# Kernel tuning notes

Hardware: AMD Instinct MI355X
Metric: run time of the kernel (lower is better)

Reference implementation:

```python
import jax, jax.numpy as jnp
import numpy as np

NUM_HEADS = 8

def _mha(x, in_w, in_b, out_w, out_b):
    # x: [B, L, E]; in_w: [3E, E]; out_w: [E, E]
    B, L, E = x.shape
    H = NUM_HEADS
    Dh = E // H
    qkv = x @ in_w.T + in_b                      # [B, L, 3E]
    q, k, v = jnp.split(qkv, 3, axis=-1)
    # [B, H, L, Dh]
    q = q.reshape(B, L, H, Dh).transpose(0, 2, 1, 3)
    k = k.reshape(B, L, H, Dh).transpose(0, 2, 1, 3)
    v = v.reshape(B, L, H, Dh).transpose(0, 2, 1, 3)
    scale = 1.0 / jnp.sqrt(jnp.asarray(Dh, dtype=x.dtype))
    scores = jnp.einsum('bhld,bhsd->bhls', q, k) * scale   # [B, H, L, S]
    attn = jax.nn.softmax(scores, axis=-1)
    ctx = jnp.einsum('bhls,bhsd->bhld', attn, v)           # [B, H, L, Dh]
    ctx = ctx.transpose(0, 2, 1, 3).reshape(B, L, E)
    out = ctx @ out_w.T + out_b                             # [B, L, E]
    # PyTorch default average_attn_weights=True: mean over heads -> [B, L, S]
    weights = attn.mean(axis=1)
    return out, weights

def setup_inputs() -> dict:
    key = jax.random.key(0)
    ks = jax.random.split(key, 5)
    B, L, E = 4, 2048, 1024
    s = 0.02
    return {
        'hidden_states': jax.random.normal(ks[0], (B, L, E), dtype=jnp.float32),
        'in_proj_w': jax.random.normal(ks[1], (3 * E, E), dtype=jnp.float32) * s,
        'in_proj_b': jnp.zeros((3 * E,), dtype=jnp.float32),
        'out_proj_w': jax.random.normal(ks[2], (E, E), dtype=jnp.float32) * s,
        'out_proj_b': jnp.zeros((E,), dtype=jnp.float32),
        'dep_proj_w': jax.random.normal(ks[3], (E, E), dtype=jnp.float32) * s,
        'dep_proj_b': jnp.zeros((E,), dtype=jnp.float32),
    }

def reference(hidden_states, in_proj_w, in_proj_b, out_proj_w, out_proj_b, dep_proj_w, dep_proj_b):
    enhanced, attn_weights = _mha(hidden_states, in_proj_w, in_proj_b, out_proj_w, out_proj_b)
    # dependency_scores: mean over query dim then key dim -> [B]
    dependency_scores = attn_weights.mean(axis=1).mean(axis=-1)
    enhanced = enhanced @ dep_proj_w.T + dep_proj_b
    return dependency_scores, enhanced
```

## Files before the change

kernel.cpp:

```cpp
#include <hip/hip_runtime.h>


typedef __attribute__((ext_vector_type(8))) short short8;
typedef __attribute__((ext_vector_type(4))) float float4v;
typedef __attribute__((ext_vector_type(4))) int int4v;
typedef __attribute__((ext_vector_type(2))) unsigned uint2v;

__device__ inline ushort f2bf(float f) {
  union { float f; unsigned u; } v; v.f = f;
  unsigned u = v.u;
  return (ushort)((u + 0x7FFFu + ((u >> 16) & 1u)) >> 16);
}
__device__ inline float bf2f(ushort h) {
  union { unsigned u; float f; } v; v.u = ((unsigned)h) << 16;
  return v.f;
}
__device__ inline unsigned cvtpk(float lo, float hi) {
  unsigned r;
  asm("v_cvt_pk_bf16_f32 %0, %1, %2" : "=v"(r) : "v"(lo), "v"(hi));
  return r;
}

__global__ __launch_bounds__(256)
void prep(const float* __restrict__ X, const float* __restrict__ Wi,
          const float* __restrict__ Wd, const float* __restrict__ Wo,
          const float* __restrict__ bo, const float* __restrict__ bd,
          ushort* __restrict__ Xb, ushort* __restrict__ Wib,
          ushort* __restrict__ Wdb, ushort* __restrict__ WoT,
          float* __restrict__ bc, float* __restrict__ dep) {
  __shared__ ushort Ts[64 * 72];
  const int bid = blockIdx.x;
  const int t = threadIdx.x;

  if (bid < 6144) {
    size_t i = ((size_t)bid * 256 + t) * 8;
    const float* src; ushort* dst;
    if (i < 8388608)        { src = X  + i;              dst = Xb  + i; }
    else if (i < 11534336)  { src = Wi + (i - 8388608);  dst = Wib + (i - 8388608); }
    else                    { src = Wd + (i - 11534336); dst = Wdb + (i - 11534336); }
    float4v a = *(const float4v*)(src);
    float4v b = *(const float4v*)(src + 4);
    ushort o[8];
    o[0] = f2bf(a.x); o[1] = f2bf(a.y); o[2] = f2bf(a.z); o[3] = f2bf(a.w);
    o[4] = f2bf(b.x); o[5] = f2bf(b.y); o[6] = f2bf(b.z); o[7] = f2bf(b.w);
    *(int4v*)dst = *(const int4v*)o;
  } else if (bid < 6400) {
    const int q = bid - 6144;
    const int ct = (q & 15) * 64, rt = (q >> 4) * 64;
#pragma unroll
    for (int i = 0; i < 4; i++) {
      const int row = i * 16 + (t >> 4), col4 = (t & 15) * 4;
      float4v v = *(const float4v*)(Wo + (size_t)(rt + row) * 1024 + ct + col4);
      ushort o[4] = {f2bf(v.x), f2bf(v.y), f2bf(v.z), f2bf(v.w)};
      *(uint2v*)(Ts + row * 72 + col4) = *(const uint2v*)o;
    }
    __syncthreads();
#pragma unroll
    for (int it = 0; it < 2; it++) {
      const int c = it * 256 + t;
      const int oc = c >> 3, r8 = (c & 7) * 8;
      ushort o[8];
#pragma unroll
      for (int j = 0; j < 8; j++) o[j] = Ts[(r8 + j) * 72 + oc];
      *(int4v*)(WoT + (size_t)(ct + oc) * 1024 + rt + r8) = *(const int4v*)o;
    }
  } else {
    const int w = t >> 6, lane = t & 63;
    const int row = (bid - 6400) * 4 + w;
    float s = 0.f;
#pragma unroll
    for (int i = 0; i < 4; i++) {
      const int j = i * 256 + lane * 4;
      float4v wv = *(const float4v*)(Wd + (size_t)row * 1024 + j);
      float4v bv = *(const float4v*)(bo + j);
      s += wv.x * bv.x + wv.y * bv.y + wv.z * bv.z + wv.w * bv.w;
    }
#pragma unroll
    for (int off = 1; off <= 32; off <<= 1) s += __shfl_xor(s, off);
    if (lane == 0) bc[row] = s + bd[row];
    if (row < 4 && lane == 1) dep[row] = 1.0f / 2048.0f;
  }
}

__global__ __launch_bounds__(256, 2)
void gemm_bt(const ushort* __restrict__ A, const ushort* __restrict__ W,
             ushort* __restrict__ C, int K) {
  __shared__ ushort As[128 * 32];
  __shared__ ushort Bs[128 * 32];
  const int t = threadIdx.x;
  const int w = t >> 6;
  const int lane = t & 63;
  const int m16 = lane & 15, quad = lane >> 4;
  const int bx = blockIdx.x, by = blockIdx.y;
  const int warpRow = w >> 1, warpCol = w & 1;

  const int srow = t >> 2;
  const int scol = (t & 3) * 8;
  const ushort* Aptr = A + (size_t)(by * 128) * K;
  const ushort* Wptr = W + (size_t)(bx * 128) * K;

  float4v zero4 = {0.f, 0.f, 0.f, 0.f};
  float4v acc[4][4];
#pragma unroll
  for (int i = 0; i < 4; i++)
#pragma unroll
    for (int j = 0; j < 4; j++) acc[i][j] = zero4;

  for (int k0 = 0; k0 < K; k0 += 32) {
    __syncthreads();
#pragma unroll
    for (int r = 0; r < 2; r++) {
      const ushort* g = Aptr + (size_t)(r * 64 + srow) * K + (k0 + scol);
      __builtin_amdgcn_global_load_lds(
          (const __attribute__((address_space(1))) void*)g,
          (__attribute__((address_space(3))) void*)(As + r * 2048 + t * 8),
          16, 0, 0);
    }
#pragma unroll
    for (int r = 0; r < 2; r++) {
      const ushort* g = Wptr + (size_t)(r * 64 + srow) * K + (k0 + scol);
      __builtin_amdgcn_global_load_lds(
          (const __attribute__((address_space(1))) void*)g,
          (__attribute__((address_space(3))) void*)(Bs + r * 2048 + t * 8),
          16, 0, 0);
    }
    __syncthreads();

    short8 af[4], bf[4];
#pragma unroll
    for (int i = 0; i < 4; i++) {
      af[i] = *(const short8*)(As + (warpRow * 64 + i * 16 + m16) * 32 + quad * 8);
      bf[i] = *(const short8*)(Bs + (warpCol * 64 + i * 16 + m16) * 32 + quad * 8);
    }
#pragma unroll
    for (int i = 0; i < 4; i++)
#pragma unroll
      for (int j = 0; j < 4; j++)
        acc[i][j] = __builtin_amdgcn_mfma_f32_16x16x32_bf16(af[i], bf[j],
                                                            acc[i][j], 0, 0, 0);
  }

  const int crow_base = by * 128 + warpRow * 64;
  const int ccol_base = bx * 128 + warpCol * 64;
#pragma unroll
  for (int j = 0; j < 4; j++) {
    const int col = ccol_base + j * 16 + m16;
#pragma unroll
    for (int i = 0; i < 4; i++) {
      const int row = crow_base + i * 16 + quad * 4;
#pragma unroll
      for (int r = 0; r < 4; r++)
        C[(size_t)(row + r) * 1024 + col] = f2bf(acc[i][j][r]);
    }
  }
}

__global__ __launch_bounds__(256, 2)
void gemm_qkv(const ushort* __restrict__ Xb, const ushort* __restrict__ Wib,
              const float* __restrict__ bi, ushort* __restrict__ qkv,
              ushort* __restrict__ Vt,
              const ushort* __restrict__ A2, const ushort* __restrict__ W2,
              ushort* __restrict__ C2) {
  __shared__ ushort As[128 * 32];
  __shared__ ushort Bs[128 * 32];
  const int t = threadIdx.x;
  const int w = t >> 6;
  const int lane = t & 63;
  const int m16 = lane & 15, quad = lane >> 4;
  const int bid = blockIdx.x;
  const bool second = bid >= 1536;
  int bx, by;
  const ushort *A, *W;
  if (!second) {
    const int swz = (bid & 7) * 192 + (bid >> 3);
    bx = swz % 24; by = swz / 24; A = Xb; W = Wib;
  } else {
    const int b2 = bid - 1536; bx = b2 & 7; by = b2 >> 3; A = A2; W = W2;
  }
  const int warpRow = w >> 1, warpCol = w & 1;
  const int K = 1024;

  const int srow = t >> 2;
  const int scol = (t & 3) * 8;
  const ushort* Aptr = A + (size_t)(by * 128) * K;
  const ushort* Wptr = W + (size_t)(bx * 128) * K;

  float4v zero4 = {0.f, 0.f, 0.f, 0.f};
  float4v acc[4][4];
#pragma unroll
  for (int i = 0; i < 4; i++)
#pragma unroll
    for (int j = 0; j < 4; j++) acc[i][j] = zero4;

  for (int k0 = 0; k0 < K; k0 += 32) {
    __syncthreads();
#pragma unroll
    for (int r = 0; r < 2; r++) {
      const ushort* g = Aptr + (size_t)(r * 64 + srow) * K + (k0 + scol);
      __builtin_amdgcn_global_load_lds(
          (const __attribute__((address_space(1))) void*)g,
          (__attribute__((address_space(3))) void*)(As + r * 2048 + t * 8),
          16, 0, 0);
    }
#pragma unroll
    for (int r = 0; r < 2; r++) {
      const ushort* g = Wptr + (size_t)(r * 64 + srow) * K + (k0 + scol);
      __builtin_amdgcn_global_load_lds(
          (const __attribute__((address_space(1))) void*)g,
          (__attribute__((address_space(3))) void*)(Bs + r * 2048 + t * 8),
          16, 0, 0);
    }
    __syncthreads();

    short8 af[4], bf[4];
#pragma unroll
    for (int i = 0; i < 4; i++) {
      af[i] = *(const short8*)(As + (warpRow * 64 + i * 16 + m16) * 32 + quad * 8);
      bf[i] = *(const short8*)(Bs + (warpCol * 64 + i * 16 + m16) * 32 + quad * 8);
    }
#pragma unroll
    for (int i = 0; i < 4; i++)
#pragma unroll
      for (int j = 0; j < 4; j++)
        acc[i][j] = __builtin_amdgcn_mfma_f32_16x16x32_bf16(af[i], bf[j],
                                                            acc[i][j], 0, 0, 0);
  }

  const int crow_base = by * 128 + warpRow * 64;
  const int ccol_base = bx * 128 + warpCol * 64;

  if (second) {
#pragma unroll
    for (int j = 0; j < 4; j++) {
      const int col = ccol_base + j * 16 + m16;
#pragma unroll
      for (int i = 0; i < 4; i++) {
        const int row = crow_base + i * 16 + quad * 4;
#pragma unroll
        for (int r = 0; r < 4; r++)
          C2[(size_t)(row + r) * 1024 + col] = f2bf(acc[i][j][r]);
      }
    }
  } else if (bx < 16) {
#pragma unroll
    for (int j = 0; j < 4; j++) {
      const int col = ccol_base + j * 16 + m16;
      const float bv = bi[col];
#pragma unroll
      for (int i = 0; i < 4; i++) {
        const int row = crow_base + i * 16 + quad * 4;
#pragma unroll
        for (int r = 0; r < 4; r++)
          qkv[(size_t)(row + r) * 3072 + col] = f2bf(acc[i][j][r] + bv);
      }
    }
  } else {
    const int b = by >> 4;
#pragma unroll
    for (int j = 0; j < 4; j++) {
      const int col = ccol_base + j * 16 + m16;
      const float bv = bi[col];
      const int vcol = col - 2048;
      const int h = vcol >> 7, d = vcol & 127;
      ushort* vrow = Vt + (size_t)((b * 8 + h) * 128 + d) * 2048;
#pragma unroll
      for (int i = 0; i < 4; i++) {
        const int pos = ((by & 15) << 7) + warpRow * 64 + ((i >> 1) << 5) +
                        (2 * quad + (i & 1)) * 4;
        uint2v o;
        o.x = cvtpk(acc[i][j][0] + bv, acc[i][j][1] + bv);
        o.y = cvtpk(acc[i][j][2] + bv, acc[i][j][3] + bv);
        *(uint2v*)(vrow + pos) = o;
      }
    }
  }
}

__global__ __launch_bounds__(512, 1)
void attn(const ushort* __restrict__ qkv, const ushort* __restrict__ Vt,
          ushort* __restrict__ ctx) {
  __shared__ ushort Ks[4][32 * 128];
  __shared__ ushort Vsm[4][128 * 32];
  const int t = threadIdx.x, w = t >> 6, lane = t & 63;
  const int m16 = lane & 15, quad = lane >> 4;
  const int i = blockIdx.x;
  const int x = i & 7, jj0 = i >> 3;
  const int pair = x * 4 + (jj0 >> 3);
  const int qt = jj0 & 7;
  const int h = pair & 7, b = pair >> 3;
  const int E3 = 3072;
  const size_t bbase = (size_t)b * 2048;

  const ushort* Qg = qkv + (bbase + qt * 256 + w * 32) * E3 + h * 128;
  const ushort* Kg = qkv + bbase * E3 + 1024 + h * 128;
  const ushort* Vg = Vt + (size_t)((b * 8 + h) * 128) * 2048;

  auto stage = [&](int kt, int buf) {
    {
      const int row = t >> 4, cir = t & 15;
      const int j = (cir & 8) | ((cir ^ row) & 7);
      const ushort* g = Kg + (size_t)(kt * 32 + row) * E3 + j * 8;
      __builtin_amdgcn_global_load_lds(
          (const __attribute__((address_space(1))) void*)g,
          (__attribute__((address_space(3))) void*)(&Ks[buf][t * 8]), 16, 0, 0);
    }
    {
      const int d = t >> 2, cir = t & 3;
      const int j = cir ^ ((d >> 1) & 3);
      const ushort* g = Vg + (size_t)d * 2048 + kt * 32 + j * 8;
      __builtin_amdgcn_global_load_lds(
          (const __attribute__((address_space(1))) void*)g,
          (__attribute__((address_space(3))) void*)(&Vsm[buf][t * 8]), 16, 0, 0);
    }
  };

  stage(0, 0);
  stage(1, 1);

  const float c1 = 0.08838834764831845f * 1.4426950408889634f;
  short8 qf[2][4];
#pragma unroll
  for (int g = 0; g < 2; g++)
#pragma unroll
    for (int ks = 0; ks < 4; ks++) {
      short8 raw = *(const short8*)(Qg + (size_t)(g * 16 + m16) * E3 + ks * 32 + quad * 8);
      short8 s;
#pragma unroll
      for (int j = 0; j < 8; j++) s[j] = (short)f2bf(bf2f((ushort)raw[j]) * c1);
      qf[g][ks] = s;
    }

  int kslot[4];
#pragma unroll
  for (int ks = 0; ks < 4; ks++) {
    const int j = ks * 4 + quad;
    kslot[ks] = (j & 8) | ((j ^ m16) & 7);
  }
  const int vslot = quad ^ ((m16 >> 1) & 3);

  float4v zero4 = {0.f, 0.f, 0.f, 0.f};
  float4v Oacc[2][8];
#pragma unroll
  for (int g = 0; g < 2; g++)
#pragma unroll
    for (int dt = 0; dt < 8; dt++) Oacc[g][dt] = zero4;
  float lsum[2] = {0.f, 0.f};

  for (int kt = 0; kt < 64; kt++) {
    if (kt < 62) {
      stage(kt + 2, (kt + 2) & 3);
      asm volatile("s_waitcnt vmcnt(4)" ::: "memory");
    } else if (kt == 62) {
      asm volatile("s_waitcnt vmcnt(2)" ::: "memory");
    } else {
      asm volatile("s_waitcnt vmcnt(0)" ::: "memory");
    }
    __builtin_amdgcn_s_barrier();
    __builtin_amdgcn_sched_barrier(0);
    const ushort* Ksb = Ks[kt & 3];
    const ushort* Vsb = Vsm[kt & 3];

    float4v st[2][2];
    st[0][0] = zero4; st[0][1] = zero4; st[1][0] = zero4; st[1][1] = zero4;
    __builtin_amdgcn_s_setprio(1);
#pragma unroll
    for (int ks = 0; ks < 4; ks++) {
#pragma unroll
      for (int mt2 = 0; mt2 < 2; mt2++) {
        short8 kf = *(const short8*)(Ksb + (mt2 * 16 + m16) * 128 + kslot[ks] * 8);
        st[0][mt2] = __builtin_amdgcn_mfma_f32_16x16x32_bf16(kf, qf[0][ks], st[0][mt2], 0, 0, 0);
        st[1][mt2] = __builtin_amdgcn_mfma_f32_16x16x32_bf16(kf, qf[1][ks], st[1][mt2], 0, 0, 0);
      }
    }
    __builtin_amdgcn_s_setprio(0);

    short8 pfr[2];
#pragma unroll
    for (int g = 0; g < 2; g++) {
      unsigned pk[4];
#pragma unroll
      for (int mt2 = 0; mt2 < 2; mt2++) {
        float p0 = __builtin_exp2f(st[g][mt2][0]);
        float p1 = __builtin_exp2f(st[g][mt2][1]);
        float p2 = __builtin_exp2f(st[g][mt2][2]);
        float p3 = __builtin_exp2f(st[g][mt2][3]);
        lsum[g] += (p0 + p1) + (p2 + p3);
        pk[mt2 * 2]     = cvtpk(p0, p1);
        pk[mt2 * 2 + 1] = cvtpk(p2, p3);
      }
      union { int4v i; short8 s; } pf;
      pf.i.x = (int)pk[0];
      pf.i.y = (int)pk[1];
      pf.i.z = (int)pk[2];
      pf.i.w = (int)pk[3];
      pfr[g] = pf.s;
    }

    __builtin_amdgcn_s_setprio(1);
#pragma unroll
    for (int dt = 0; dt < 8; dt++) {
      short8 vf = *(const short8*)(Vsb + (dt * 16 + m16) * 32 + vslot * 8);
      Oacc[0][dt] = __builtin_amdgcn_mfma_f32_16x16x32_bf16(pfr[0], vf, Oacc[0][dt], 0, 0, 0);
      Oacc[1][dt] = __builtin_amdgcn_mfma_f32_16x16x32_bf16(pfr[1], vf, Oacc[1][dt], 0, 0, 0);
    }
    __builtin_amdgcn_s_setprio(0);
  }

#pragma unroll
  for (int g = 0; g < 2; g++) {
    float l = lsum[g];
    l += __shfl_xor(l, 16);
    l += __shfl_xor(l, 32);
    float* lf = (float*)(&Ks[0][w * 64]);
    lf[m16] = l;
    float linv[4];
#pragma unroll
    for (int r = 0; r < 4; r++) linv[r] = 1.0f / lf[quad * 4 + r];
#pragma unroll
    for (int r = 0; r < 4; r++) {
      const int row = qt * 256 + w * 32 + g * 16 + quad * 4 + r;
      ushort* crow = ctx + (bbase + row) * 1024 + h * 128;
#pragma unroll
      for (int dt = 0; dt < 8; dt++)
        crow[dt * 16 + m16] = f2bf(Oacc[g][dt][r] * linv[r]);
    }
  }
}

__global__ __launch_bounds__(256, 2)
void gemm_fin(const ushort* __restrict__ A, const ushort* __restrict__ W,
              const float* __restrict__ bias, float* __restrict__ C) {
  __shared__ ushort As[128 * 32];
  __shared__ ushort Bs[128 * 32];
  const int t = threadIdx.x;
  const int w = t >> 6;
  const int lane = t & 63;
  const int m16 = lane & 15, quad = lane >> 4;
  const int swz = (blockIdx.x & 7) * 64 + (blockIdx.x >> 3);
  const int bx = swz & 7, by = swz >> 3;
  const int warpRow = w >> 1, warpCol = w & 1;
  const int K = 1024;

  const int srow = t >> 2;
  const int scol = (t & 3) * 8;
  const ushort* Aptr = A + (size_t)(by * 128) * K;
  const ushort* Wptr = W + (size_t)(bx * 128) * K;

  float4v zero4 = {0.f, 0.f, 0.f, 0.f};
  float4v acc[4][4];
#pragma unroll
  for (int i = 0; i < 4; i++)
#pragma unroll
    for (int j = 0; j < 4; j++) acc[i][j] = zero4;

  for (int k0 = 0; k0 < K; k0 += 32) {
    __syncthreads();
#pragma unroll
    for (int r = 0; r < 2; r++) {
      const ushort* g = Aptr + (size_t)(r * 64 + srow) * K + (k0 + scol);
      __builtin_amdgcn_global_load_lds(
          (const __attribute__((address_space(1))) void*)g,
          (__attribute__((address_space(3))) void*)(As + r * 2048 + t * 8),
          16, 0, 0);
    }
#pragma unroll
    for (int r = 0; r < 2; r++) {
      const ushort* g = Wptr + (size_t)(r * 64 + srow) * K + (k0 + scol);
      __builtin_amdgcn_global_load_lds(
          (const __attribute__((address_space(1))) void*)g,
          (__attribute__((address_space(3))) void*)(Bs + r * 2048 + t * 8),
          16, 0, 0);
    }
    __syncthreads();

    short8 af[4], bf[4];
#pragma unroll
    for (int i = 0; i < 4; i++) {
      af[i] = *(const short8*)(As + (warpRow * 64 + i * 16 + m16) * 32 + quad * 8);
      bf[i] = *(const short8*)(Bs + (warpCol * 64 + i * 16 + m16) * 32 + quad * 8);
    }
#pragma unroll
    for (int i = 0; i < 4; i++)
#pragma unroll
      for (int j = 0; j < 4; j++)
        acc[i][j] = __builtin_amdgcn_mfma_f32_16x16x32_bf16(af[i], bf[j],
                                                            acc[i][j], 0, 0, 0);
  }

  const int crow_base = by * 128 + warpRow * 64;
  const int ccol_base = bx * 128 + warpCol * 64;
#pragma unroll
  for (int j = 0; j < 4; j++) {
    const int col = ccol_base + j * 16 + m16;
    const float bv = bias[col];
#pragma unroll
    for (int i = 0; i < 4; i++) {
      const int row = crow_base + i * 16 + quad * 4;
#pragma unroll
      for (int r = 0; r < 4; r++)
        C[(size_t)(row + r) * 1024 + col] = acc[i][j][r] + bv;
    }
  }
}

extern "C" void kernel_launch(void* const* d_in, const int* in_sizes, int n_in,
                              void* d_out, int out_size, void* d_ws, size_t ws_size,
                              hipStream_t stream) {
  const float* X  = (const float*)d_in[0];
  const float* Wi = (const float*)d_in[1];
  const float* bi = (const float*)d_in[2];
  const float* Wo = (const float*)d_in[3];
  const float* bo = (const float*)d_in[4];
  const float* Wd = (const float*)d_in[5];
  const float* bd = (const float*)d_in[6];
  float* out = (float*)d_out;

  ushort* p    = (ushort*)d_ws;
  ushort* Xb   = p; p += (size_t)8192 * 1024;
  ushort* Wib  = p; p += (size_t)3072 * 1024;
  ushort* WoTb = p; p += (size_t)1024 * 1024;
  ushort* Wdb  = p; p += (size_t)1024 * 1024;
  ushort* qkv  = p; p += (size_t)8192 * 3072;
  ushort* Vt   = p; p += (size_t)4096 * 2048;
  float*  bc   = (float*)p; p += 2048;
  ushort* WcbSep = p; p += (size_t)1024 * 1024;
  const size_t need_merged = (size_t)((char*)p - (char*)d_ws);
  const bool merged = ws_size >= need_merged;

  ushort* ctx = Xb;
  ushort* Wcb = merged ? WcbSep : Wib;

  prep<<<6656, 256, 0, stream>>>(X, Wi, Wd, Wo, bo, bd,
                                 Xb, Wib, Wdb, WoTb, bc, out);
  if (merged) {
    gemm_qkv<<<1600, 256, 0, stream>>>(Xb, Wib, bi, qkv, Vt, Wdb, WoTb, Wcb);
  } else {
    gemm_qkv<<<1536, 256, 0, stream>>>(Xb, Wib, bi, qkv, Vt, Wdb, WoTb, nullptr);
    gemm_bt<<<dim3(8, 8), 256, 0, stream>>>(Wdb, WoTb, Wcb, 1024);
  }
  attn<<<256, 512, 0, stream>>>(qkv, Vt, ctx);
  gemm_fin<<<512, 256, 0, stream>>>(ctx, Wcb, bc, out + 4);
}
```

Baseline: 287.3 us.

## Restructure attention into 2-wave blocks with 64 query rows per wave

The attention kernel goes from 512-thread blocks of 8 waves, each handling 32 query rows, to 128-thread blocks of 2 waves, each handling 64 query rows. The grid doubles to 512 blocks. Each wave now reuses every K and V fragment loaded from LDS across four query groups instead of two, and each thread issues four times as many async global-to-LDS loads per stage, so the vmcnt waits are raised to match. This cuts LDS read traffic per MFMA and spreads work over more blocks, at the cost of more registers (larger Q and O accumulators) and fewer waves per block to hide latency.

```diff
diff --git a/kernel.cpp b/kernel.cpp
--- a/kernel.cpp
+++ b/kernel.cpp
@@ -276,7 +276,7 @@
   }
 }
 
-__global__ __launch_bounds__(512, 1)
+__global__ __launch_bounds__(128, 1)
 void attn(const ushort* __restrict__ qkv, const ushort* __restrict__ Vt,
           ushort* __restrict__ ctx) {
   __shared__ ushort Ks[4][32 * 128];
@@ -284,33 +284,37 @@
   const int t = threadIdx.x, w = t >> 6, lane = t & 63;
   const int m16 = lane & 15, quad = lane >> 4;
   const int i = blockIdx.x;
-  const int x = i & 7, jj0 = i >> 3;
-  const int pair = x * 4 + (jj0 >> 3);
-  const int qt = jj0 & 7;
+  const int x = i & 7, r0 = i >> 3;
+  const int pair = x * 4 + (r0 >> 4);
+  const int qt = r0 & 15;
   const int h = pair & 7, b = pair >> 3;
   const int E3 = 3072;
   const size_t bbase = (size_t)b * 2048;
 
-  const ushort* Qg = qkv + (bbase + qt * 256 + w * 32) * E3 + h * 128;
+  const ushort* Qg = qkv + (bbase + qt * 128 + w * 64) * E3 + h * 128;
   const ushort* Kg = qkv + bbase * E3 + 1024 + h * 128;
   const ushort* Vg = Vt + (size_t)((b * 8 + h) * 128) * 2048;
 
   auto stage = [&](int kt, int buf) {
-    {
-      const int row = t >> 4, cir = t & 15;
+#pragma unroll
+    for (int it = 0; it < 4; it++) {
+      const int c = it * 128 + t;
+      const int row = c >> 4, cir = c & 15;
       const int j = (cir & 8) | ((cir ^ row) & 7);
       const ushort* g = Kg + (size_t)(kt * 32 + row) * E3 + j * 8;
       __builtin_amdgcn_global_load_lds(
           (const __attribute__((address_space(1))) void*)g,
-          (__attribute__((address_space(3))) void*)(&Ks[buf][t * 8]), 16, 0, 0);
-    }
-    {
-      const int d = t >> 2, cir = t & 3;
+          (__attribute__((address_space(3))) void*)(&Ks[buf][c * 8]), 16, 0, 0);
+    }
+#pragma unroll
+    for (int it = 0; it < 4; it++) {
+      const int c = it * 128 + t;
+      const int d = c >> 2, cir = c & 3;
       const int j = cir ^ ((d >> 1) & 3);
       const ushort* g = Vg + (size_t)d * 2048 + kt * 32 + j * 8;
       __builtin_amdgcn_global_load_lds(
           (const __attribute__((address_space(1))) void*)g,
-          (__attribute__((address_space(3))) void*)(&Vsm[buf][t * 8]), 16, 0, 0);
+          (__attribute__((address_space(3))) void*)(&Vsm[buf][c * 8]), 16, 0, 0);
     }
   };
 
@@ -318,9 +322,9 @@
   stage(1, 1);
 
   const float c1 = 0.08838834764831845f * 1.4426950408889634f;
-  short8 qf[2][4];
-#pragma unroll
-  for (int g = 0; g < 2; g++)
+  short8 qf[4][4];
+#pragma unroll
+  for (int g = 0; g < 4; g++)
 #pragma unroll
     for (int ks = 0; ks < 4; ks++) {
       short8 raw = *(const short8*)(Qg + (size_t)(g * 16 + m16) * E3 + ks * 32 + quad * 8);
@@ -339,19 +343,19 @@
   const int vslot = quad ^ ((m16 >> 1) & 3);
 
   float4v zero4 = {0.f, 0.f, 0.f, 0.f};
-  float4v Oacc[2][8];
-#pragma unroll
-  for (int g = 0; g < 2; g++)
+  float4v Oacc[4][8];
+#pragma unroll
+  for (int g = 0; g < 4; g++)
 #pragma unroll
     for (int dt = 0; dt < 8; dt++) Oacc[g][dt] = zero4;
-  float lsum[2] = {0.f, 0.f};
+  float lsum[4] = {0.f, 0.f, 0.f, 0.f};
 
   for (int kt = 0; kt < 64; kt++) {
     if (kt < 62) {
       stage(kt + 2, (kt + 2) & 3);
-      asm volatile("s_waitcnt vmcnt(4)" ::: "memory");
+      asm volatile("s_waitcnt vmcnt(16)" ::: "memory");
     } else if (kt == 62) {
-      asm volatile("s_waitcnt vmcnt(2)" ::: "memory");
+      asm volatile("s_waitcnt vmcnt(8)" ::: "memory");
     } else {
       asm volatile("s_waitcnt vmcnt(0)" ::: "memory");
     }
@@ -360,23 +364,25 @@
     const ushort* Ksb = Ks[kt & 3];
     const ushort* Vsb = Vsm[kt & 3];
 
-    float4v st[2][2];
-    st[0][0] = zero4; st[0][1] = zero4; st[1][0] = zero4; st[1][1] = zero4;
+    float4v st[4][2];
+#pragma unroll
+    for (int g = 0; g < 4; g++) { st[g][0] = zero4; st[g][1] = zero4; }
     __builtin_amdgcn_s_setprio(1);
 #pragma unroll
     for (int ks = 0; ks < 4; ks++) {
 #pragma unroll
       for (int mt2 = 0; mt2 < 2; mt2++) {
         short8 kf = *(const short8*)(Ksb + (mt2 * 16 + m16) * 128 + kslot[ks] * 8);
-        st[0][mt2] = __builtin_amdgcn_mfma_f32_16x16x32_bf16(kf, qf[0][ks], st[0][mt2], 0, 0, 0);
-        st[1][mt2] = __builtin_amdgcn_mfma_f32_16x16x32_bf16(kf, qf[1][ks], st[1][mt2], 0, 0, 0);
+#pragma unroll
+        for (int g = 0; g < 4; g++)
+          st[g][mt2] = __builtin_amdgcn_mfma_f32_16x16x32_bf16(kf, qf[g][ks], st[g][mt2], 0, 0, 0);
       }
     }
     __builtin_amdgcn_s_setprio(0);
 
-    short8 pfr[2];
-#pragma unroll
-    for (int g = 0; g < 2; g++) {
+    short8 pfr[4];
+#pragma unroll
+    for (int g = 0; g < 4; g++) {
       unsigned pk[4];
 #pragma unroll
       for (int mt2 = 0; mt2 < 2; mt2++) {
@@ -400,14 +406,15 @@
 #pragma unroll
     for (int dt = 0; dt < 8; dt++) {
       short8 vf = *(const short8*)(Vsb + (dt * 16 + m16) * 32 + vslot * 8);
-      Oacc[0][dt] = __builtin_amdgcn_mfma_f32_16x16x32_bf16(pfr[0], vf, Oacc[0][dt], 0, 0, 0);
-      Oacc[1][dt] = __builtin_amdgcn_mfma_f32_16x16x32_bf16(pfr[1], vf, Oacc[1][dt], 0, 0, 0);
+#pragma unroll
+      for (int g = 0; g < 4; g++)
+        Oacc[g][dt] = __builtin_amdgcn_mfma_f32_16x16x32_bf16(pfr[g], vf, Oacc[g][dt], 0, 0, 0);
     }
     __builtin_amdgcn_s_setprio(0);
   }
 
 #pragma unroll
-  for (int g = 0; g < 2; g++) {
+  for (int g = 0; g < 4; g++) {
     float l = lsum[g];
     l += __shfl_xor(l, 16);
     l += __shfl_xor(l, 32);
@@ -418,7 +425,7 @@
     for (int r = 0; r < 4; r++) linv[r] = 1.0f / lf[quad * 4 + r];
 #pragma unroll
     for (int r = 0; r < 4; r++) {
-      const int row = qt * 256 + w * 32 + g * 16 + quad * 4 + r;
+      const int row = qt * 128 + w * 64 + g * 16 + quad * 4 + r;
       ushort* crow = ctx + (bbase + row) * 1024 + h * 128;
 #pragma unroll
       for (int dt = 0; dt < 8; dt++)
@@ -538,6 +545,6 @@
     gemm_qkv<<<1536, 256, 0, stream>>>(Xb, Wib, bi, qkv, Vt, Wdb, WoTb, nullptr);
     gemm_bt<<<dim3(8, 8), 256, 0, stream>>>(Wdb, WoTb, Wcb, 1024);
   }
-  attn<<<256, 512, 0, stream>>>(qkv, Vt, ctx);
+  attn<<<512, 128, 0, stream>>>(qkv, Vt, ctx);
   gemm_fin<<<512, 256, 0, stream>>>(ctx, Wcb, bc, out + 4);
 }
```

New measurement: 310.6 us. 1.08x slower.

## Replace LDS-staged attention with single-wave blocks loading K/V directly into registers

Applied to the files above, without the earlier changes.

The attention kernel moves from 512-thread blocks that share K/V tiles through a 4-deep LDS ring with barriers to 64-thread single-wave blocks. Each wave now loads its own K and V fragments from global memory into registers, prefetching the next tile (K double-buffered, V reloaded after use), and the row-sum broadcast uses shuffles instead of LDS. This removes block barriers and LDS traffic. In exchange, every wave re-reads the full K/V for its head, raising global and L2 traffic about eightfold, and it adds register pressure.

```diff
diff --git a/kernel.cpp b/kernel.cpp
--- a/kernel.cpp
+++ b/kernel.cpp
@@ -276,46 +276,37 @@
   }
 }
 
-__global__ __launch_bounds__(512, 1)
+__global__ __launch_bounds__(64, 2)
 void attn(const ushort* __restrict__ qkv, const ushort* __restrict__ Vt,
           ushort* __restrict__ ctx) {
-  __shared__ ushort Ks[4][32 * 128];
-  __shared__ ushort Vsm[4][128 * 32];
-  const int t = threadIdx.x, w = t >> 6, lane = t & 63;
+  const int lane = threadIdx.x;
   const int m16 = lane & 15, quad = lane >> 4;
   const int i = blockIdx.x;
-  const int x = i & 7, jj0 = i >> 3;
-  const int pair = x * 4 + (jj0 >> 3);
-  const int qt = jj0 & 7;
+  const int x = i & 7, j0 = i >> 3;
+  const int pair = x * 4 + (j0 >> 6);
+  const int qw = j0 & 63;
   const int h = pair & 7, b = pair >> 3;
   const int E3 = 3072;
   const size_t bbase = (size_t)b * 2048;
 
-  const ushort* Qg = qkv + (bbase + qt * 256 + w * 32) * E3 + h * 128;
+  const ushort* Qg = qkv + (bbase + qw * 32) * E3 + h * 128;
   const ushort* Kg = qkv + bbase * E3 + 1024 + h * 128;
   const ushort* Vg = Vt + (size_t)((b * 8 + h) * 128) * 2048;
 
-  auto stage = [&](int kt, int buf) {
-    {
-      const int row = t >> 4, cir = t & 15;
-      const int j = (cir & 8) | ((cir ^ row) & 7);
-      const ushort* g = Kg + (size_t)(kt * 32 + row) * E3 + j * 8;
-      __builtin_amdgcn_global_load_lds(
-          (const __attribute__((address_space(1))) void*)g,
-          (__attribute__((address_space(3))) void*)(&Ks[buf][t * 8]), 16, 0, 0);
-    }
-    {
-      const int d = t >> 2, cir = t & 3;
-      const int j = cir ^ ((d >> 1) & 3);
-      const ushort* g = Vg + (size_t)d * 2048 + kt * 32 + j * 8;
-      __builtin_amdgcn_global_load_lds(
-          (const __attribute__((address_space(1))) void*)g,
-          (__attribute__((address_space(3))) void*)(&Vsm[buf][t * 8]), 16, 0, 0);
-    }
+  auto loadK = [&](int kt, short8* kf) {
+#pragma unroll
+    for (int mt2 = 0; mt2 < 2; mt2++)
+#pragma unroll
+      for (int ks = 0; ks < 4; ks++)
+        kf[mt2 * 4 + ks] = *(const short8*)(
+            Kg + (size_t)(kt * 32 + mt2 * 16 + m16) * E3 + ks * 32 + quad * 8);
   };
-
-  stage(0, 0);
-  stage(1, 1);
+  auto loadV = [&](int kt, short8* vf) {
+#pragma unroll
+    for (int dt = 0; dt < 8; dt++)
+      vf[dt] = *(const short8*)(
+          Vg + (size_t)(dt * 16 + m16) * 2048 + kt * 32 + quad * 8);
+  };
 
   const float c1 = 0.08838834764831845f * 1.4426950408889634f;
   short8 qf[2][4];
@@ -326,17 +317,14 @@
       short8 raw = *(const short8*)(Qg + (size_t)(g * 16 + m16) * E3 + ks * 32 + quad * 8);
       short8 s;
 #pragma unroll
-      for (int j = 0; j < 8; j++) s[j] = (short)f2bf(bf2f((ushort)raw[j]) * c1);
+      for (int jj = 0; jj < 8; jj++) s[jj] = (short)f2bf(bf2f((ushort)raw[jj]) * c1);
       qf[g][ks] = s;
     }
 
-  int kslot[4];
-#pragma unroll
-  for (int ks = 0; ks < 4; ks++) {
-    const int j = ks * 4 + quad;
-    kslot[ks] = (j & 8) | ((j ^ m16) & 7);
-  }
-  const int vslot = quad ^ ((m16 >> 1) & 3);
+  short8 kf[2][8];
+  short8 vfr[8];
+  loadK(0, kf[0]);
+  loadV(0, vfr);
 
   float4v zero4 = {0.f, 0.f, 0.f, 0.f};
   float4v Oacc[2][8];
@@ -346,19 +334,9 @@
     for (int dt = 0; dt < 8; dt++) Oacc[g][dt] = zero4;
   float lsum[2] = {0.f, 0.f};
 
+#pragma unroll 2
   for (int kt = 0; kt < 64; kt++) {
-    if (kt < 62) {
-      stage(kt + 2, (kt + 2) & 3);
-      asm volatile("s_waitcnt vmcnt(4)" ::: "memory");
-    } else if (kt == 62) {
-      asm volatile("s_waitcnt vmcnt(2)" ::: "memory");
-    } else {
-      asm volatile("s_waitcnt vmcnt(0)" ::: "memory");
-    }
-    __builtin_amdgcn_s_barrier();
-    __builtin_amdgcn_sched_barrier(0);
-    const ushort* Ksb = Ks[kt & 3];
-    const ushort* Vsb = Vsm[kt & 3];
+    const int cur = kt & 1;
 
     float4v st[2][2];
     st[0][0] = zero4; st[0][1] = zero4; st[1][0] = zero4; st[1][1] = zero4;
@@ -367,12 +345,14 @@
     for (int ks = 0; ks < 4; ks++) {
 #pragma unroll
       for (int mt2 = 0; mt2 < 2; mt2++) {
-        short8 kf = *(const short8*)(Ksb + (mt2 * 16 + m16) * 128 + kslot[ks] * 8);
-        st[0][mt2] = __builtin_amdgcn_mfma_f32_16x16x32_bf16(kf, qf[0][ks], st[0][mt2], 0, 0, 0);
-        st[1][mt2] = __builtin_amdgcn_mfma_f32_16x16x32_bf16(kf, qf[1][ks], st[1][mt2], 0, 0, 0);
+        st[0][mt2] = __builtin_amdgcn_mfma_f32_16x16x32_bf16(
+            kf[cur][mt2 * 4 + ks], qf[0][ks], st[0][mt2], 0, 0, 0);
+        st[1][mt2] = __builtin_amdgcn_mfma_f32_16x16x32_bf16(
+            kf[cur][mt2 * 4 + ks], qf[1][ks], st[1][mt2], 0, 0, 0);
       }
     }
     __builtin_amdgcn_s_setprio(0);
+    if (kt < 63) loadK(kt + 1, kf[cur ^ 1]);
 
     short8 pfr[2];
 #pragma unroll
@@ -388,22 +368,22 @@
         pk[mt2 * 2]     = cvtpk(p0, p1);
         pk[mt2 * 2 + 1] = cvtpk(p2, p3);
       }
-      union { int4v i; short8 s; } pf;
-      pf.i.x = (int)pk[0];
-      pf.i.y = (int)pk[1];
-      pf.i.z = (int)pk[2];
-      pf.i.w = (int)pk[3];
+      union { int4v iv; short8 s; } pf;
+      pf.iv.x = (int)pk[0];
+      pf.iv.y = (int)pk[1];
+      pf.iv.z = (int)pk[2];
+      pf.iv.w = (int)pk[3];
       pfr[g] = pf.s;
     }
 
     __builtin_amdgcn_s_setprio(1);
 #pragma unroll
     for (int dt = 0; dt < 8; dt++) {
-      short8 vf = *(const short8*)(Vsb + (dt * 16 + m16) * 32 + vslot * 8);
-      Oacc[0][dt] = __builtin_amdgcn_mfma_f32_16x16x32_bf16(pfr[0], vf, Oacc[0][dt], 0, 0, 0);
-      Oacc[1][dt] = __builtin_amdgcn_mfma_f32_16x16x32_bf16(pfr[1], vf, Oacc[1][dt], 0, 0, 0);
+      Oacc[0][dt] = __builtin_amdgcn_mfma_f32_16x16x32_bf16(pfr[0], vfr[dt], Oacc[0][dt], 0, 0, 0);
+      Oacc[1][dt] = __builtin_amdgcn_mfma_f32_16x16x32_bf16(pfr[1], vfr[dt], Oacc[1][dt], 0, 0, 0);
     }
     __builtin_amdgcn_s_setprio(0);
+    if (kt < 63) loadV(kt + 1, vfr);
   }
 
 #pragma unroll
@@ -411,14 +391,12 @@
     float l = lsum[g];
     l += __shfl_xor(l, 16);
     l += __shfl_xor(l, 32);
-    float* lf = (float*)(&Ks[0][w * 64]);
-    lf[m16] = l;
     float linv[4];
 #pragma unroll
-    for (int r = 0; r < 4; r++) linv[r] = 1.0f / lf[quad * 4 + r];
+    for (int r = 0; r < 4; r++) linv[r] = 1.0f / __shfl(l, quad * 4 + r);
 #pragma unroll
     for (int r = 0; r < 4; r++) {
-      const int row = qt * 256 + w * 32 + g * 16 + quad * 4 + r;
+      const int row = qw * 32 + g * 16 + quad * 4 + r;
       ushort* crow = ctx + (bbase + row) * 1024 + h * 128;
 #pragma unroll
       for (int dt = 0; dt < 8; dt++)
@@ -538,6 +516,6 @@
     gemm_qkv<<<1536, 256, 0, stream>>>(Xb, Wib, bi, qkv, Vt, Wdb, WoTb, nullptr);
     gemm_bt<<<dim3(8, 8), 256, 0, stream>>>(Wdb, WoTb, Wcb, 1024);
   }
-  attn<<<256, 512, 0, stream>>>(qkv, Vt, ctx);
+  attn<<<2048, 64, 0, stream>>>(qkv, Vt, ctx);
   gemm_fin<<<512, 256, 0, stream>>>(ctx, Wcb, bc, out + 4);
 }
```

After: 430.5 us. 1.5x slower.

## Split attention blocks to 256 threads with two blocks per CU

Applied to the files above, without the earlier changes.

The attention kernel now runs with 256-thread blocks covering 128 query rows instead of 512-thread blocks covering 256 rows, launching 512 blocks with a launch bound of two blocks per CU. Each thread issues two async K and V loads per stage, and the vmcnt waits are raised to match. The aim is better CU fill (512 blocks against 256 CUs) and overlap between co-resident blocks. In exchange, each K/V tile is loaded from global memory twice as often across the grid, since fewer queries share each staged tile.

```diff
diff --git a/kernel.cpp b/kernel.cpp
--- a/kernel.cpp
+++ b/kernel.cpp
@@ -276,7 +276,7 @@
   }
 }
 
-__global__ __launch_bounds__(512, 1)
+__global__ __launch_bounds__(256, 2)
 void attn(const ushort* __restrict__ qkv, const ushort* __restrict__ Vt,
           ushort* __restrict__ ctx) {
   __shared__ ushort Ks[4][32 * 128];
@@ -284,33 +284,37 @@
   const int t = threadIdx.x, w = t >> 6, lane = t & 63;
   const int m16 = lane & 15, quad = lane >> 4;
   const int i = blockIdx.x;
-  const int x = i & 7, jj0 = i >> 3;
-  const int pair = x * 4 + (jj0 >> 3);
-  const int qt = jj0 & 7;
+  const int x = i & 7, r0 = i >> 3;
+  const int pair = x * 4 + (r0 >> 4);
+  const int qt = r0 & 15;
   const int h = pair & 7, b = pair >> 3;
   const int E3 = 3072;
   const size_t bbase = (size_t)b * 2048;
 
-  const ushort* Qg = qkv + (bbase + qt * 256 + w * 32) * E3 + h * 128;
+  const ushort* Qg = qkv + (bbase + qt * 128 + w * 32) * E3 + h * 128;
   const ushort* Kg = qkv + bbase * E3 + 1024 + h * 128;
   const ushort* Vg = Vt + (size_t)((b * 8 + h) * 128) * 2048;
 
   auto stage = [&](int kt, int buf) {
-    {
-      const int row = t >> 4, cir = t & 15;
+#pragma unroll
+    for (int it = 0; it < 2; it++) {
+      const int c = it * 256 + t;
+      const int row = c >> 4, cir = c & 15;
       const int j = (cir & 8) | ((cir ^ row) & 7);
       const ushort* g = Kg + (size_t)(kt * 32 + row) * E3 + j * 8;
       __builtin_amdgcn_global_load_lds(
           (const __attribute__((address_space(1))) void*)g,
-          (__attribute__((address_space(3))) void*)(&Ks[buf][t * 8]), 16, 0, 0);
-    }
-    {
-      const int d = t >> 2, cir = t & 3;
+          (__attribute__((address_space(3))) void*)(&Ks[buf][c * 8]), 16, 0, 0);
+    }
+#pragma unroll
+    for (int it = 0; it < 2; it++) {
+      const int c = it * 256 + t;
+      const int d = c >> 2, cir = c & 3;
       const int j = cir ^ ((d >> 1) & 3);
       const ushort* g = Vg + (size_t)d * 2048 + kt * 32 + j * 8;
       __builtin_amdgcn_global_load_lds(
           (const __attribute__((address_space(1))) void*)g,
-          (__attribute__((address_space(3))) void*)(&Vsm[buf][t * 8]), 16, 0, 0);
+          (__attribute__((address_space(3))) void*)(&Vsm[buf][c * 8]), 16, 0, 0);
     }
   };
 
@@ -349,9 +353,9 @@
   for (int kt = 0; kt < 64; kt++) {
     if (kt < 62) {
       stage(kt + 2, (kt + 2) & 3);
+      asm volatile("s_waitcnt vmcnt(8)" ::: "memory");
+    } else if (kt == 62) {
       asm volatile("s_waitcnt vmcnt(4)" ::: "memory");
-    } else if (kt == 62) {
-      asm volatile("s_waitcnt vmcnt(2)" ::: "memory");
     } else {
       asm volatile("s_waitcnt vmcnt(0)" ::: "memory");
     }
@@ -388,11 +392,11 @@
         pk[mt2 * 2]     = cvtpk(p0, p1);
         pk[mt2 * 2 + 1] = cvtpk(p2, p3);
       }
-      union { int4v i; short8 s; } pf;
-      pf.i.x = (int)pk[0];
-      pf.i.y = (int)pk[1];
-      pf.i.z = (int)pk[2];
-      pf.i.w = (int)pk[3];
+      union { int4v iv; short8 s; } pf;
+      pf.iv.x = (int)pk[0];
+      pf.iv.y = (int)pk[1];
+      pf.iv.z = (int)pk[2];
+      pf.iv.w = (int)pk[3];
       pfr[g] = pf.s;
     }
 
@@ -418,7 +422,7 @@
     for (int r = 0; r < 4; r++) linv[r] = 1.0f / lf[quad * 4 + r];
 #pragma unroll
     for (int r = 0; r < 4; r++) {
-      const int row = qt * 256 + w * 32 + g * 16 + quad * 4 + r;
+      const int row = qt * 128 + w * 32 + g * 16 + quad * 4 + r;
       ushort* crow = ctx + (bbase + row) * 1024 + h * 128;
 #pragma unroll
       for (int dt = 0; dt < 8; dt++)
@@ -538,6 +542,6 @@
     gemm_qkv<<<1536, 256, 0, stream>>>(Xb, Wib, bi, qkv, Vt, Wdb, WoTb, nullptr);
     gemm_bt<<<dim3(8, 8), 256, 0, stream>>>(Wdb, WoTb, Wcb, 1024);
   }
-  attn<<<256, 512, 0, stream>>>(qkv, Vt, ctx);
+  attn<<<512, 256, 0, stream>>>(qkv, Vt, ctx);
   gemm_fin<<<512, 256, 0, stream>>>(ctx, Wcb, bc, out + 4);
 }
```

Measured after the change: 283.9 us. About the same (-1.2%).
